# Optimization experiments

Measured on AMD Instinct MI355X. Metric: run time of the kernel, lower is better.

The kernel has to match this reference:

```python
import jax, jax.numpy as jnp
import numpy as np

NUM_HEADS = 8
KEY_DIM = 16
D_V = 32  # attn_ratio * key_dim


def _conv1x1_bn(x, w, s, b):
    # x: [B, Cin, H, W], w: [Cout, Cin]; 1x1 conv == channel contraction,
    # eval-mode BatchNorm folded into per-channel scale s and bias b.
    y = jnp.einsum('bchw,oc->bohw', x, w)
    return y * s[:, None, None] + b[:, None, None]


def setup_inputs() -> dict:
    key = jax.random.key(0)
    ks = jax.random.split(key, 14)
    B, C, H, W = 16, 256, 32, 32
    nh_kd, dh = NUM_HEADS * KEY_DIM, NUM_HEADS * D_V
    f = jax.random.normal
    return {
        'x': f(ks[0], (B, C, H, W), jnp.float32),
        'wq': f(ks[1], (nh_kd, C), jnp.float32) * 0.05,
        'sq': jax.random.uniform(ks[2], (nh_kd,), jnp.float32),
        'bq': f(ks[3], (nh_kd,), jnp.float32) * 0.05,
        'wk': f(ks[4], (nh_kd, C), jnp.float32) * 0.05,
        'sk': jax.random.uniform(ks[5], (nh_kd,), jnp.float32),
        'bk': f(ks[6], (nh_kd,), jnp.float32) * 0.05,
        'wv': f(ks[7], (dh, C), jnp.float32) * 0.05,
        'sv': jax.random.uniform(ks[8], (dh,), jnp.float32),
        'bv': f(ks[9], (dh,), jnp.float32) * 0.05,
        'wp': f(ks[10], (C, dh), jnp.float32) * 0.05,
        'sp': jax.random.uniform(ks[11], (C,), jnp.float32),
        'bp': f(ks[12], (C,), jnp.float32) * 0.05,
    }


def reference(x, wq, sq, bq, wk, sk, bk, wv, sv, bv, wp, sp, bp):
    B, C, H, W = x.shape
    N = H * W
    # QKV projections (1x1 conv + folded BN)
    q = _conv1x1_bn(x, wq, sq, bq).reshape(B, NUM_HEADS, KEY_DIM, N)  # b h k n
    k = _conv1x1_bn(x, wk, sk, bk).reshape(B, NUM_HEADS, KEY_DIM, N)  # b h k m
    v = _conv1x1_bn(x, wv, sv, bv).reshape(B, NUM_HEADS, D_V, N)      # b h d m
    # NOTE: the original forward does NOT apply self.scale to the scores.
    attn = jnp.einsum('bhkn,bhkm->bhnm', q, k)
    attn = jax.nn.softmax(attn, axis=-1)
    out = jnp.einsum('bhnm,bhdm->bhdn', attn, v)  # b h d n
    out = out.reshape(B, NUM_HEADS * D_V, H, W)
    # proj = Sequential(activation, Conv2d_BN): activation FIRST
    out = jax.nn.relu(out)
    return _conv1x1_bn(out, wp, sp, bp)
```

## Files before the change

### kernel.cpp

```cpp
#include <hip/hip_runtime.h>

#define NTOT 1024
#define CIN  256
#define BATCH 16
#define NH   8
#define KD   16
#define DV   32
#define L2E  1.44269504088896340736f

typedef unsigned short u16;
typedef unsigned int   u32;
typedef __attribute__((ext_vector_type(2)))  _Float16 f16x2;
typedef __attribute__((ext_vector_type(8)))  _Float16 f16x8;
typedef __attribute__((ext_vector_type(16))) float    f32x16;

__device__ inline f16x8 as_f16x8(uint4 u) { return __builtin_bit_cast(f16x8, u); }
__device__ inline f16x2 as_f16x2(u32 u)   { return __builtin_bit_cast(f16x2, u); }
__device__ inline u32 pkrtz(float a, float b) {
  return __builtin_bit_cast(u32, __builtin_amdgcn_cvt_pkrtz(a, b));
}
__device__ inline u16 f2h(float x) {
  return __builtin_bit_cast(u16, (_Float16)x);
}
__device__ inline float fexp2(float x) {
#if __has_builtin(__builtin_amdgcn_exp2f)
  return __builtin_amdgcn_exp2f(x);
#else
  float r; asm("v_exp_f32 %0, %1" : "=v"(r) : "v"(x)); return r;
#endif
}
__device__ inline float dot2acc(u32 p2, float c) {
#if __has_builtin(__builtin_amdgcn_fdot2)
  const f16x2 one2 = __builtin_bit_cast(f16x2, (u32)0x3C003C00u);
  return __builtin_amdgcn_fdot2(as_f16x2(p2), one2, c, false);
#else
  const f16x2 v = as_f16x2(p2);
  return c + (float)v[0] + (float)v[1];
#endif
}

__global__ __launch_bounds__(256) void prep_fused(
    const float* __restrict__ X, u16* __restrict__ Xt,
    const float* __restrict__ wq, const float* __restrict__ sq, const float* __restrict__ bq,
    const float* __restrict__ wk, const float* __restrict__ sk, const float* __restrict__ bk,
    const float* __restrict__ wv, const float* __restrict__ sv, const float* __restrict__ bv,
    const float* __restrict__ wp, const float* __restrict__ sp, const float* __restrict__ bp,
    u16* __restrict__ wqkv, u16* __restrict__ wph, float* __restrict__ ball)
{
  __shared__ u16 T[64][64];
  const int bx = blockIdx.x;
  const int t  = threadIdx.x;
  if (bx < 1024) {
    const int n0 = (bx & 15) * 64;
    const int c0 = ((bx >> 4) & 3) * 64;
    const int b  = bx >> 6;
    #pragma unroll
    for (int rr = 0; rr < 4; ++rr) {
      const int c  = rr*16 + (t>>4);
      const int n4 = (t&15)*4;
      const float4 v = *(const float4*)&X[((size_t)b*CIN + c0 + c)*NTOT + n0 + n4];
      ushort4 r; r.x=f2h(v.x); r.y=f2h(v.y); r.z=f2h(v.z); r.w=f2h(v.w);
      *(ushort4*)&T[c][n4] = r;
    }
    __syncthreads();
    const int nl = t & 63;
    #pragma unroll
    for (int j = 0; j < 2; ++j) {
      const int oct = (t>>6)*2 + j;
      uint4 w;
      w.x = (u32)T[oct*8+0][nl] | ((u32)T[oct*8+1][nl] << 16);
      w.y = (u32)T[oct*8+2][nl] | ((u32)T[oct*8+3][nl] << 16);
      w.z = (u32)T[oct*8+4][nl] | ((u32)T[oct*8+5][nl] << 16);
      w.w = (u32)T[oct*8+6][nl] | ((u32)T[oct*8+7][nl] << 16);
      *(uint4*)&Xt[((size_t)b*NTOT + n0 + nl)*CIN + c0 + oct*8] = w;
    }
  } else {
    const int row = (bx - 1024)*4 + (t>>6);
    const int ln  = t & 63;
    const float* src; u16* dst; float sc, bi;
    if (row < 128)      { src = wq + (size_t)row*CIN;       sc = sq[row]*L2E;     bi = bq[row]*L2E;     dst = wqkv + (size_t)row*CIN; }
    else if (row < 256) { src = wk + (size_t)(row-128)*CIN; sc = sk[row-128];     bi = bk[row-128];     dst = wqkv + (size_t)row*CIN; }
    else if (row < 512) { src = wv + (size_t)(row-256)*CIN; sc = sv[row-256];     bi = bv[row-256];     dst = wqkv + (size_t)row*CIN; }
    else                { src = wp + (size_t)(row-512)*CIN; sc = sp[row-512];     bi = bp[row-512];     dst = wph + (size_t)(row-512)*CIN; }
    const float4 v = *(const float4*)&src[ln*4];
    ushort4 r;
    r.x = f2h(v.x*sc); r.y = f2h(v.y*sc); r.z = f2h(v.z*sc); r.w = f2h(v.w*sc);
    *(ushort4*)&dst[ln*4] = r;
    if (ln == 0) ball[row] = bi;
  }
}

template<int BN, int MODE>
__global__ __launch_bounds__(256) void conv_mfma(
    const u16* __restrict__ Wh, const u16* __restrict__ Bt,
    const float* __restrict__ ball,
    u16* __restrict__ q_t, u16* __restrict__ k_t, u16* __restrict__ v_h,
    float* __restrict__ outp)
{
  constexpr int FN = BN / 64;
  constexpr int NB = BN / 32;
  __shared__ u16 A_lds[2][128 * 64];
  __shared__ u16 B_lds[2][BN * 64];
  const int t    = threadIdx.x;
  const int lane = t & 63;
  const int w    = t >> 6;
  const int wm = w >> 1, wn = w & 1;
  const int g = lane >> 5, nl = lane & 31;
  const int n0 = blockIdx.x * BN;
  const int m0 = blockIdx.y * 128;
  const int b  = blockIdx.z;

  f32x16 acc[2][FN] = {};
  uint4 rA[4], rB[NB];

  #pragma unroll
  for (int r = 0; r < 4; ++r) {
    const int idx = t + r*256, row = idx >> 3, ch = idx & 7;
    rA[r] = *(const uint4*)&Wh[(size_t)(m0+row)*CIN + ch*8];
  }
  #pragma unroll
  for (int r = 0; r < NB; ++r) {
    const int idx = t + r*256, row = idx >> 3, ch = idx & 7;
    rB[r] = *(const uint4*)&Bt[((size_t)b*NTOT + n0 + row)*CIN + ch*8];
  }
  #pragma unroll
  for (int r = 0; r < 4; ++r) {
    const int idx = t + r*256, row = idx >> 3, ch = idx & 7;
    *(uint4*)&A_lds[0][row*64 + ((ch ^ (row&7))*8)] = rA[r];
  }
  #pragma unroll
  for (int r = 0; r < NB; ++r) {
    const int idx = t + r*256, row = idx >> 3, ch = idx & 7;
    *(uint4*)&B_lds[0][row*64 + ((ch ^ (row&7))*8)] = rB[r];
  }
  __syncthreads();

  for (int it = 0; it < 4; ++it) {
    const int cur = it & 1;
    if (it < 3) {
      const int c0 = (it+1)*64;
      #pragma unroll
      for (int r = 0; r < 4; ++r) {
        const int idx = t + r*256, row = idx >> 3, ch = idx & 7;
        rA[r] = *(const uint4*)&Wh[(size_t)(m0+row)*CIN + c0 + ch*8];
      }
      #pragma unroll
      for (int r = 0; r < NB; ++r) {
        const int idx = t + r*256, row = idx >> 3, ch = idx & 7;
        rB[r] = *(const uint4*)&Bt[((size_t)b*NTOT + n0 + row)*CIN + c0 + ch*8];
      }
    }
    #pragma unroll
    for (int ks = 0; ks < 4; ++ks) {
      const int ch = 2*ks + g;
      f16x8 a[2], bb[FN];
      #pragma unroll
      for (int fi = 0; fi < 2; ++fi) {
        const int row = wm*64 + fi*32 + nl;
        a[fi] = as_f16x8(*(const uint4*)&A_lds[cur][row*64 + ((ch ^ (row&7))*8)]);
      }
      #pragma unroll
      for (int fj = 0; fj < FN; ++fj) {
        const int row = wn*(BN/2) + fj*32 + nl;
        bb[fj] = as_f16x8(*(const uint4*)&B_lds[cur][row*64 + ((ch ^ (row&7))*8)]);
      }
      #pragma unroll
      for (int fi = 0; fi < 2; ++fi)
        #pragma unroll
        for (int fj = 0; fj < FN; ++fj)
          acc[fi][fj] = __builtin_amdgcn_mfma_f32_32x32x16_f16(a[fi], bb[fj], acc[fi][fj], 0, 0, 0);
    }
    if (it < 3) {
      #pragma unroll
      for (int r = 0; r < 4; ++r) {
        const int idx = t + r*256, row = idx >> 3, ch = idx & 7;
        *(uint4*)&A_lds[cur^1][row*64 + ((ch ^ (row&7))*8)] = rA[r];
      }
      #pragma unroll
      for (int r = 0; r < NB; ++r) {
        const int idx = t + r*256, row = idx >> 3, ch = idx & 7;
        *(uint4*)&B_lds[cur^1][row*64 + ((ch ^ (row&7))*8)] = rB[r];
      }
      __syncthreads();
    }
  }

  #pragma unroll
  for (int fi = 0; fi < 2; ++fi) {
    #pragma unroll
    for (int fj = 0; fj < FN; ++fj) {
      const int n = n0 + wn*(BN/2) + fj*32 + nl;
      #pragma unroll
      for (int q = 0; q < 4; ++q) {
        const int ob = m0 + wm*64 + fi*32 + 8*q + 4*g;
        const float v0 = acc[fi][fj][4*q+0] + ball[ob+0];
        const float v1 = acc[fi][fj][4*q+1] + ball[ob+1];
        const float v2 = acc[fi][fj][4*q+2] + ball[ob+2];
        const float v3 = acc[fi][fj][4*q+3] + ball[ob+3];
        if (MODE == 0) {
          if (ob < 128) {
            const int h = ob >> 4, k0 = ob & 15;
            ushort4 r; r.x = f2h(v0); r.y = f2h(v1); r.z = f2h(v2); r.w = f2h(v3);
            *(ushort4*)&q_t[(((size_t)b*NH + h)*NTOT + n)*KD + k0] = r;
          } else if (ob < 256) {
            const int oo = ob - 128;
            const int h = oo >> 4, k0 = oo & 15;
            const int plane = k0 >> 3, j0 = k0 & 7;
            ushort4 r; r.x = f2h(v0); r.y = f2h(v1); r.z = f2h(v2); r.w = f2h(v3);
            *(ushort4*)&k_t[((((size_t)b*NH + h)*2 + plane)*NTOT + n)*8 + j0] = r;
          } else {
            const int oo = ob - 256;
            const int h = oo >> 5, d0 = oo & 31;
            const int mb = n >> 4, loc = n & 15;
            const int g2 = (loc >> 2) & 1;
            const int j  = (loc & 3) + ((loc >> 3) << 2);
            u16* vp = v_h + (((((size_t)b*NH + h)*64 + mb)*2 + g2)*32 + d0)*8 + j;
            vp[0*8] = f2h(v0);
            vp[1*8] = f2h(v1);
            vp[2*8] = f2h(v2);
            vp[3*8] = f2h(v3);
          }
        } else {
          float* op = outp + ((size_t)b*CIN + ob)*NTOT + n;
          op[0*NTOT] = v0; op[1*NTOT] = v1; op[2*NTOT] = v2; op[3*NTOT] = v3;
        }
      }
    }
  }
}

__global__ __launch_bounds__(1024) void attn_mfma(
    const u16* __restrict__ Qt,
    const u16* __restrict__ Kt,
    const u16* __restrict__ Vt,
    u16* __restrict__ Ot)
{
  __shared__ u16 K_lds[2*NTOT*8];
  __shared__ u16 V_lds[4096*8];
  const int t    = threadIdx.x;
  const int lane = t & 63;
  const int wave = t >> 6;
  const int bh   = blockIdx.x >> 1;
  const int half = blockIdx.x & 1;
  const int g = lane >> 5, nl = lane & 31;
  const int n0 = half*512 + wave*32;

  const u16* Kh = Kt + (size_t)bh*(2*NTOT*8);
  const u16* Vh = Vt + (size_t)bh*(4096*8);
  const u16* Qh = Qt + (size_t)bh*(NTOT*KD);

  #pragma unroll
  for (int r = 0; r < 2; ++r) {
    const int uu = r*1024 + t;
    *(uint4*)&K_lds[uu*8] = *(const uint4*)&Kh[uu*8];
  }
  #pragma unroll
  for (int r = 0; r < 4; ++r) {
    const int uu = r*1024 + t;
    *(uint4*)&V_lds[uu*8] = *(const uint4*)&Vh[uu*8];
  }

  const f16x8 qf = as_f16x8(*(const uint4*)&Qh[(size_t)(n0+nl)*KD + g*8]);
  __syncthreads();

  const f32x16 fzero = {};
  f32x16 acc = {};
  float l = 0.f;
  const char* Kb = (const char*)K_lds + g*16384 + nl*16;
  const char* Vb = (const char*)V_lds + g*512   + nl*16;

  f16x8 kf  = as_f16x8(*(const uint4*)(Kb));
  uint4 va0 = *(const uint4*)(Vb);
  uint4 va1 = *(const uint4*)(Vb + 1024);
  f32x16 s_cur = __builtin_amdgcn_mfma_f32_32x32x16_f16(kf, qf, fzero, 0, 0, 0);

  #pragma unroll 2
  for (int st = 0; st < 31; ++st) {
    const f16x8 kfn = as_f16x8(*(const uint4*)(Kb + (st+1)*512));
    __builtin_amdgcn_s_setprio(1);
    const f32x16 s_next = __builtin_amdgcn_mfma_f32_32x32x16_f16(kfn, qf, fzero, 0, 0, 0);
    __builtin_amdgcn_s_setprio(0);
    const uint4 nva0 = *(const uint4*)(Vb + (st+1)*2048);
    const uint4 nva1 = *(const uint4*)(Vb + (st+1)*2048 + 1024);

    float p[16];
    #pragma unroll
    for (int r = 0; r < 16; ++r) p[r] = fexp2(s_cur[r]);
    uint4 b0, b1;
    b0.x = pkrtz(p[0],  p[1]);  b0.y = pkrtz(p[2],  p[3]);
    b0.z = pkrtz(p[4],  p[5]);  b0.w = pkrtz(p[6],  p[7]);
    b1.x = pkrtz(p[8],  p[9]);  b1.y = pkrtz(p[10], p[11]);
    b1.z = pkrtz(p[12], p[13]); b1.w = pkrtz(p[14], p[15]);
    l = dot2acc(b0.x, l); l = dot2acc(b0.y, l);
    l = dot2acc(b0.z, l); l = dot2acc(b0.w, l);
    l = dot2acc(b1.x, l); l = dot2acc(b1.y, l);
    l = dot2acc(b1.z, l); l = dot2acc(b1.w, l);

    __builtin_amdgcn_s_setprio(1);
    acc = __builtin_amdgcn_mfma_f32_32x32x16_f16(as_f16x8(va0), as_f16x8(b0), acc, 0, 0, 0);
    acc = __builtin_amdgcn_mfma_f32_32x32x16_f16(as_f16x8(va1), as_f16x8(b1), acc, 0, 0, 0);
    __builtin_amdgcn_s_setprio(0);
    s_cur = s_next; va0 = nva0; va1 = nva1;
  }
  {
    float p[16];
    #pragma unroll
    for (int r = 0; r < 16; ++r) p[r] = fexp2(s_cur[r]);
    uint4 b0, b1;
    b0.x = pkrtz(p[0],  p[1]);  b0.y = pkrtz(p[2],  p[3]);
    b0.z = pkrtz(p[4],  p[5]);  b0.w = pkrtz(p[6],  p[7]);
    b1.x = pkrtz(p[8],  p[9]);  b1.y = pkrtz(p[10], p[11]);
    b1.z = pkrtz(p[12], p[13]); b1.w = pkrtz(p[14], p[15]);
    l = dot2acc(b0.x, l); l = dot2acc(b0.y, l);
    l = dot2acc(b0.z, l); l = dot2acc(b0.w, l);
    l = dot2acc(b1.x, l); l = dot2acc(b1.y, l);
    l = dot2acc(b1.z, l); l = dot2acc(b1.w, l);
    acc = __builtin_amdgcn_mfma_f32_32x32x16_f16(as_f16x8(va0), as_f16x8(b0), acc, 0, 0, 0);
    acc = __builtin_amdgcn_mfma_f32_32x32x16_f16(as_f16x8(va1), as_f16x8(b1), acc, 0, 0, 0);
  }

  const float lt = l + __shfl_xor(l, 32);
  const float rl = 1.0f / lt;
  const int b = bh >> 3, h = bh & 7;
  u16* op = Ot + ((size_t)b*NTOT + n0 + nl)*CIN + h*DV;
  #pragma unroll
  for (int q = 0; q < 4; ++q) {
    const float v0 = fmaxf(acc[4*q+0]*rl, 0.f);
    const float v1 = fmaxf(acc[4*q+1]*rl, 0.f);
    const float v2 = fmaxf(acc[4*q+2]*rl, 0.f);
    const float v3 = fmaxf(acc[4*q+3]*rl, 0.f);
    uint2 pk; pk.x = pkrtz(v0, v1); pk.y = pkrtz(v2, v3);
    *(uint2*)&op[8*q + 4*g] = pk;
  }
}

extern "C" void kernel_launch(void* const* d_in, const int* in_sizes, int n_in,
                              void* d_out, int out_size, void* d_ws, size_t ws_size,
                              hipStream_t stream) {
  const float* x  = (const float*)d_in[0];
  const float* wq = (const float*)d_in[1];
  const float* sq = (const float*)d_in[2];
  const float* bq = (const float*)d_in[3];
  const float* wk = (const float*)d_in[4];
  const float* sk = (const float*)d_in[5];
  const float* bk = (const float*)d_in[6];
  const float* wv = (const float*)d_in[7];
  const float* sv = (const float*)d_in[8];
  const float* bv = (const float*)d_in[9];
  const float* wp = (const float*)d_in[10];
  const float* sp = (const float*)d_in[11];
  const float* bp = (const float*)d_in[12];
  float* out = (float*)d_out;

  char* ws = (char*)d_ws;
  u16*   x_t  = (u16*)(ws);
  u16*   q_t  = (u16*)(ws + (8u  << 20));
  u16*   k_t  = (u16*)(ws + (12u << 20));
  u16*   v_h  = (u16*)(ws + (16u << 20));
  u16*   wqkv = (u16*)(ws + (24u << 20));
  u16*   wph  = (u16*)(ws + (24u << 20) + (256u << 10));
  float* ball = (float*)(ws + (24u << 20) + (384u << 10));

  prep_fused<<<dim3(1216), dim3(256), 0, stream>>>(
      x, x_t, wq, sq, bq, wk, sk, bk, wv, sv, bv, wp, sp, bp, wqkv, wph, ball);
  conv_mfma<128, 0><<<dim3(8, 4, 16), dim3(256), 0, stream>>>(
      wqkv, x_t, ball, q_t, k_t, v_h, nullptr);
  attn_mfma<<<dim3(256), dim3(1024), 0, stream>>>(q_t, k_t, v_h, x_t );
  conv_mfma<64, 1><<<dim3(16, 2, 16), dim3(256), 0, stream>>>(
      wph, x_t , ball + 512, nullptr, nullptr, nullptr, out);
}
```

Before: 57.08 us.

## Split attention keys across wave pairs and stream V through double-buffered LDS

The attention kernel now launches 1024 blocks of 512 threads instead of 256 blocks of 1024. Each block covers 128 queries, and the key range is split between two wave groups whose partial accumulators and row sums are merged through LDS at the end. V is no longer loaded whole up front. It is staged chunk by chunk into a double-buffered LDS area with a barrier per chunk, which shrinks LDS use so more blocks can be resident and lets loading overlap with compute. The row sum also uses four independent accumulators to shorten the dependency chain. The cost is that K is reloaded four times more often overall, plus extra barriers and a final reduction step.

Result: slower. 102.6 us (+79.7%).

```diff
diff --git a/kernel.cpp b/kernel.cpp
--- a/kernel.cpp
+++ b/kernel.cpp
@@ -229,108 +229,121 @@
   }
 }
 
-__global__ __launch_bounds__(1024) void attn_mfma(
+#define ATTN_STEP(SLOC, DO_NEXT, DO_KF)                                  \
+  {                                                                      \
+    const uint4 va0 = *(const uint4*)&vbuf[((SLOC)&1)*1024 + g*256 + nl*8];       \
+    const uint4 va1 = *(const uint4*)&vbuf[((SLOC)&1)*1024 + 512 + g*256 + nl*8]; \
+    f32x16 s_next;                                                       \
+    if (DO_NEXT) {                                                       \
+      __builtin_amdgcn_s_setprio(1);                                     \
+      s_next = __builtin_amdgcn_mfma_f32_32x32x16_f16(kf, qf, fzero, 0, 0, 0); \
+      __builtin_amdgcn_s_setprio(0);                                     \
+    }                                                                    \
+    if (DO_KF) kf = as_f16x8(*(const uint4*)(Kb + ((SLOC)+2)*512));      \
+    float p[16];                                                         \
+    _Pragma("unroll")                                                    \
+    for (int r = 0; r < 16; ++r) p[r] = fexp2(s_cur[r]);                 \
+    uint4 pb0, pb1;                                                      \
+    pb0.x = pkrtz(p[0],  p[1]);  pb0.y = pkrtz(p[2],  p[3]);             \
+    pb0.z = pkrtz(p[4],  p[5]);  pb0.w = pkrtz(p[6],  p[7]);             \
+    pb1.x = pkrtz(p[8],  p[9]);  pb1.y = pkrtz(p[10], p[11]);            \
+    pb1.z = pkrtz(p[12], p[13]); pb1.w = pkrtz(p[14], p[15]);            \
+    l0 = dot2acc(pb0.x, l0); l1 = dot2acc(pb0.y, l1);                    \
+    l2 = dot2acc(pb0.z, l2); l3 = dot2acc(pb0.w, l3);                    \
+    l0 = dot2acc(pb1.x, l0); l1 = dot2acc(pb1.y, l1);                    \
+    l2 = dot2acc(pb1.z, l2); l3 = dot2acc(pb1.w, l3);                    \
+    __builtin_amdgcn_s_setprio(1);                                       \
+    acc = __builtin_amdgcn_mfma_f32_32x32x16_f16(as_f16x8(va0), as_f16x8(pb0), acc, 0, 0, 0); \
+    acc = __builtin_amdgcn_mfma_f32_32x32x16_f16(as_f16x8(va1), as_f16x8(pb1), acc, 0, 0, 0); \
+    __builtin_amdgcn_s_setprio(0);                                       \
+    if (DO_NEXT) s_cur = s_next;                                         \
+  }
+
+__global__ __launch_bounds__(512, 6) void attn_mfma(
     const u16* __restrict__ Qt,
     const u16* __restrict__ Kt,
     const u16* __restrict__ Vt,
     u16* __restrict__ Ot)
 {
   __shared__ u16 K_lds[2*NTOT*8];
-  __shared__ u16 V_lds[4096*8];
+  __shared__ u16 V_lds[2][2][2048];
   const int t    = threadIdx.x;
   const int lane = t & 63;
-  const int wave = t >> 6;
-  const int bh   = blockIdx.x >> 1;
-  const int half = blockIdx.x & 1;
+  const int w    = t >> 6;
+  const int qg   = w & 3;
+  const int mh   = w >> 2;
+  const int bh    = blockIdx.x >> 3;
+  const int qpart = blockIdx.x & 7;
   const int g = lane >> 5, nl = lane & 31;
-  const int n0 = half*512 + wave*32;
+  const int n0 = qpart*128 + qg*32;
 
   const u16* Kh = Kt + (size_t)bh*(2*NTOT*8);
   const u16* Vh = Vt + (size_t)bh*(4096*8);
   const u16* Qh = Qt + (size_t)bh*(NTOT*KD);
 
   #pragma unroll
-  for (int r = 0; r < 2; ++r) {
-    const int uu = r*1024 + t;
+  for (int r = 0; r < 4; ++r) {
+    const int uu = r*512 + t;
     *(uint4*)&K_lds[uu*8] = *(const uint4*)&Kh[uu*8];
   }
-  #pragma unroll
-  for (int r = 0; r < 4; ++r) {
-    const int uu = r*1024 + t;
-    *(uint4*)&V_lds[uu*8] = *(const uint4*)&Vh[uu*8];
-  }
+  const int sh   = t >> 8;
+  const int sidx = t & 255;
+  const u16* Vsrc = Vh + sh*16384 + sidx*8;
+  *(uint4*)&V_lds[sh][0][sidx*8] = *(const uint4*)(Vsrc);
 
   const f16x8 qf = as_f16x8(*(const uint4*)&Qh[(size_t)(n0+nl)*KD + g*8]);
   __syncthreads();
 
   const f32x16 fzero = {};
   f32x16 acc = {};
-  float l = 0.f;
-  const char* Kb = (const char*)K_lds + g*16384 + nl*16;
-  const char* Vb = (const char*)V_lds + g*512   + nl*16;
-
-  f16x8 kf  = as_f16x8(*(const uint4*)(Kb));
-  uint4 va0 = *(const uint4*)(Vb);
-  uint4 va1 = *(const uint4*)(Vb + 1024);
+  float l0 = 0.f, l1 = 0.f, l2 = 0.f, l3 = 0.f;
+  const char* Kb = (const char*)K_lds + g*16384 + mh*8192 + nl*16;
+
+  f16x8 kf = as_f16x8(*(const uint4*)(Kb));
   f32x16 s_cur = __builtin_amdgcn_mfma_f32_32x32x16_f16(kf, qf, fzero, 0, 0, 0);
-
-  #pragma unroll 2
-  for (int st = 0; st < 31; ++st) {
-    const f16x8 kfn = as_f16x8(*(const uint4*)(Kb + (st+1)*512));
-    __builtin_amdgcn_s_setprio(1);
-    const f32x16 s_next = __builtin_amdgcn_mfma_f32_32x32x16_f16(kfn, qf, fzero, 0, 0, 0);
-    __builtin_amdgcn_s_setprio(0);
-    const uint4 nva0 = *(const uint4*)(Vb + (st+1)*2048);
-    const uint4 nva1 = *(const uint4*)(Vb + (st+1)*2048 + 1024);
-
-    float p[16];
-    #pragma unroll
-    for (int r = 0; r < 16; ++r) p[r] = fexp2(s_cur[r]);
-    uint4 b0, b1;
-    b0.x = pkrtz(p[0],  p[1]);  b0.y = pkrtz(p[2],  p[3]);
-    b0.z = pkrtz(p[4],  p[5]);  b0.w = pkrtz(p[6],  p[7]);
-    b1.x = pkrtz(p[8],  p[9]);  b1.y = pkrtz(p[10], p[11]);
-    b1.z = pkrtz(p[12], p[13]); b1.w = pkrtz(p[14], p[15]);
-    l = dot2acc(b0.x, l); l = dot2acc(b0.y, l);
-    l = dot2acc(b0.z, l); l = dot2acc(b0.w, l);
-    l = dot2acc(b1.x, l); l = dot2acc(b1.y, l);
-    l = dot2acc(b1.z, l); l = dot2acc(b1.w, l);
-
-    __builtin_amdgcn_s_setprio(1);
-    acc = __builtin_amdgcn_mfma_f32_32x32x16_f16(as_f16x8(va0), as_f16x8(b0), acc, 0, 0, 0);
-    acc = __builtin_amdgcn_mfma_f32_32x32x16_f16(as_f16x8(va1), as_f16x8(b1), acc, 0, 0, 0);
-    __builtin_amdgcn_s_setprio(0);
-    s_cur = s_next; va0 = nva0; va1 = nva1;
+  kf = as_f16x8(*(const uint4*)(Kb + 512));
+
+  for (int c = 0; c < 7; ++c) {
+    const uint4 vstage = *(const uint4*)(Vsrc + (size_t)(c+1)*2048);
+    const u16* vbuf = &V_lds[mh][c & 1][0];
+    ATTN_STEP(2*c,     true, true);
+    ATTN_STEP(2*c + 1, true, true);
+    *(uint4*)&V_lds[sh][(c & 1) ^ 1][sidx*8] = vstage;
+    __syncthreads();
   }
   {
-    float p[16];
-    #pragma unroll
-    for (int r = 0; r < 16; ++r) p[r] = fexp2(s_cur[r]);
-    uint4 b0, b1;
-    b0.x = pkrtz(p[0],  p[1]);  b0.y = pkrtz(p[2],  p[3]);
-    b0.z = pkrtz(p[4],  p[5]);  b0.w = pkrtz(p[6],  p[7]);
-    b1.x = pkrtz(p[8],  p[9]);  b1.y = pkrtz(p[10], p[11]);
-    b1.z = pkrtz(p[12], p[13]); b1.w = pkrtz(p[14], p[15]);
-    l = dot2acc(b0.x, l); l = dot2acc(b0.y, l);
-    l = dot2acc(b0.z, l); l = dot2acc(b0.w, l);
-    l = dot2acc(b1.x, l); l = dot2acc(b1.y, l);
-    l = dot2acc(b1.z, l); l = dot2acc(b1.w, l);
-    acc = __builtin_amdgcn_mfma_f32_32x32x16_f16(as_f16x8(va0), as_f16x8(b0), acc, 0, 0, 0);
-    acc = __builtin_amdgcn_mfma_f32_32x32x16_f16(as_f16x8(va1), as_f16x8(b1), acc, 0, 0, 0);
-  }
-
-  const float lt = l + __shfl_xor(l, 32);
-  const float rl = 1.0f / lt;
-  const int b = bh >> 3, h = bh & 7;
-  u16* op = Ot + ((size_t)b*NTOT + n0 + nl)*CIN + h*DV;
-  #pragma unroll
-  for (int q = 0; q < 4; ++q) {
-    const float v0 = fmaxf(acc[4*q+0]*rl, 0.f);
-    const float v1 = fmaxf(acc[4*q+1]*rl, 0.f);
-    const float v2 = fmaxf(acc[4*q+2]*rl, 0.f);
-    const float v3 = fmaxf(acc[4*q+3]*rl, 0.f);
-    uint2 pk; pk.x = pkrtz(v0, v1); pk.y = pkrtz(v2, v3);
-    *(uint2*)&op[8*q + 4*g] = pk;
+    const u16* vbuf = &V_lds[mh][1][0];
+    ATTN_STEP(14, true,  false);
+    ATTN_STEP(15, false, false);
+  }
+
+  __syncthreads();
+  float* M = (float*)K_lds;
+  const int mo = qg * 1088;
+  const float lp = (l0 + l1) + (l2 + l3);
+  if (mh == 0) {
+    #pragma unroll
+    for (int r = 0; r < 16; ++r) M[mo + r*64 + lane] = acc[r];
+    M[mo + 1024 + lane] = lp;
+  }
+  __syncthreads();
+  if (mh == 1) {
+    #pragma unroll
+    for (int r = 0; r < 16; ++r) acc[r] += M[mo + r*64 + lane];
+    const float lsum = lp + M[mo + 1024 + lane];
+    const float lt = lsum + __shfl_xor(lsum, 32);
+    const float rl = 1.0f / lt;
+    const int b = bh >> 3, h = bh & 7;
+    u16* op = Ot + ((size_t)b*NTOT + n0 + nl)*CIN + h*DV;
+    #pragma unroll
+    for (int q = 0; q < 4; ++q) {
+      const float v0 = fmaxf(acc[4*q+0]*rl, 0.f);
+      const float v1 = fmaxf(acc[4*q+1]*rl, 0.f);
+      const float v2 = fmaxf(acc[4*q+2]*rl, 0.f);
+      const float v3 = fmaxf(acc[4*q+3]*rl, 0.f);
+      uint2 pk; pk.x = pkrtz(v0, v1); pk.y = pkrtz(v2, v3);
+      *(uint2*)&op[8*q + 4*g] = pk;
+    }
   }
 }
 
@@ -365,7 +378,7 @@
       x, x_t, wq, sq, bq, wk, sk, bk, wv, sv, bv, wp, sp, bp, wqkv, wph, ball);
   conv_mfma<128, 0><<<dim3(8, 4, 16), dim3(256), 0, stream>>>(
       wqkv, x_t, ball, q_t, k_t, v_h, nullptr);
-  attn_mfma<<<dim3(256), dim3(1024), 0, stream>>>(q_t, k_t, v_h, x_t );
+  attn_mfma<<<dim3(1024), dim3(512), 0, stream>>>(q_t, k_t, v_h, x_t );
   conv_mfma<64, 1><<<dim3(16, 2, 16), dim3(256), 0, stream>>>(
       wph, x_t , ball + 512, nullptr, nullptr, nullptr, out);
 }
```

## Fuse X transpose into QKV conv, restructure attention loop, remap blocks

Applied to the files above, without the earlier changes.

Removes the separate fp32→fp16 transpose of X by having the QKV conv read X directly and scatter-convert it into swizzled LDS, dropping a global round trip for the transposed copy. The conv loses its register double-buffering and now uses single-buffered LDS with scalar 16-bit LDS stores. The attention kernel is restructured into a two-stream unrolled loop with four independent row-sum accumulators to expose more MFMA/exp overlap, and its block index is remapped so that consecutive blocks span different batch-heads. The weight prep becomes its own small kernel.

New measurement: 133.9 us. 2.35x slower.

```diff
diff --git a/kernel.cpp b/kernel.cpp
--- a/kernel.cpp
+++ b/kernel.cpp
@@ -39,157 +39,93 @@
 #endif
 }
 
-__global__ __launch_bounds__(256) void prep_fused(
-    const float* __restrict__ X, u16* __restrict__ Xt,
+__global__ __launch_bounds__(64) void prep_weights(
     const float* __restrict__ wq, const float* __restrict__ sq, const float* __restrict__ bq,
     const float* __restrict__ wk, const float* __restrict__ sk, const float* __restrict__ bk,
     const float* __restrict__ wv, const float* __restrict__ sv, const float* __restrict__ bv,
     const float* __restrict__ wp, const float* __restrict__ sp, const float* __restrict__ bp,
     u16* __restrict__ wqkv, u16* __restrict__ wph, float* __restrict__ ball)
 {
-  __shared__ u16 T[64][64];
-  const int bx = blockIdx.x;
-  const int t  = threadIdx.x;
-  if (bx < 1024) {
-    const int n0 = (bx & 15) * 64;
-    const int c0 = ((bx >> 4) & 3) * 64;
-    const int b  = bx >> 6;
-    #pragma unroll
-    for (int rr = 0; rr < 4; ++rr) {
-      const int c  = rr*16 + (t>>4);
-      const int n4 = (t&15)*4;
-      const float4 v = *(const float4*)&X[((size_t)b*CIN + c0 + c)*NTOT + n0 + n4];
-      ushort4 r; r.x=f2h(v.x); r.y=f2h(v.y); r.z=f2h(v.z); r.w=f2h(v.w);
-      *(ushort4*)&T[c][n4] = r;
-    }
-    __syncthreads();
-    const int nl = t & 63;
-    #pragma unroll
-    for (int j = 0; j < 2; ++j) {
-      const int oct = (t>>6)*2 + j;
-      uint4 w;
-      w.x = (u32)T[oct*8+0][nl] | ((u32)T[oct*8+1][nl] << 16);
-      w.y = (u32)T[oct*8+2][nl] | ((u32)T[oct*8+3][nl] << 16);
-      w.z = (u32)T[oct*8+4][nl] | ((u32)T[oct*8+5][nl] << 16);
-      w.w = (u32)T[oct*8+6][nl] | ((u32)T[oct*8+7][nl] << 16);
-      *(uint4*)&Xt[((size_t)b*NTOT + n0 + nl)*CIN + c0 + oct*8] = w;
-    }
-  } else {
-    const int row = (bx - 1024)*4 + (t>>6);
-    const int ln  = t & 63;
-    const float* src; u16* dst; float sc, bi;
-    if (row < 128)      { src = wq + (size_t)row*CIN;       sc = sq[row]*L2E;     bi = bq[row]*L2E;     dst = wqkv + (size_t)row*CIN; }
-    else if (row < 256) { src = wk + (size_t)(row-128)*CIN; sc = sk[row-128];     bi = bk[row-128];     dst = wqkv + (size_t)row*CIN; }
-    else if (row < 512) { src = wv + (size_t)(row-256)*CIN; sc = sv[row-256];     bi = bv[row-256];     dst = wqkv + (size_t)row*CIN; }
-    else                { src = wp + (size_t)(row-512)*CIN; sc = sp[row-512];     bi = bp[row-512];     dst = wph + (size_t)(row-512)*CIN; }
-    const float4 v = *(const float4*)&src[ln*4];
-    ushort4 r;
-    r.x = f2h(v.x*sc); r.y = f2h(v.y*sc); r.z = f2h(v.z*sc); r.w = f2h(v.w*sc);
-    *(ushort4*)&dst[ln*4] = r;
-    if (ln == 0) ball[row] = bi;
-  }
-}
-
-template<int BN, int MODE>
-__global__ __launch_bounds__(256) void conv_mfma(
-    const u16* __restrict__ Wh, const u16* __restrict__ Bt,
+  const int row = blockIdx.x;
+  const int t = threadIdx.x;
+  const float* src; u16* dst; float sc, bi;
+  if (row < 128)      { src = wq + (size_t)row*CIN;       sc = sq[row]*L2E;     bi = bq[row]*L2E;     dst = wqkv + (size_t)row*CIN; }
+  else if (row < 256) { src = wk + (size_t)(row-128)*CIN; sc = sk[row-128];     bi = bk[row-128];     dst = wqkv + (size_t)row*CIN; }
+  else if (row < 512) { src = wv + (size_t)(row-256)*CIN; sc = sv[row-256];     bi = bv[row-256];     dst = wqkv + (size_t)row*CIN; }
+  else                { src = wp + (size_t)(row-512)*CIN; sc = sp[row-512];     bi = bp[row-512];     dst = wph + (size_t)(row-512)*CIN; }
+  const float4 v = *(const float4*)&src[t*4];
+  ushort4 r;
+  r.x = f2h(v.x*sc); r.y = f2h(v.y*sc); r.z = f2h(v.z*sc); r.w = f2h(v.w*sc);
+  *(ushort4*)&dst[t*4] = r;
+  if (t == 0) ball[row] = bi;
+}
+
+__global__ __launch_bounds__(256) void conv_qkv(
+    const float* __restrict__ X, const u16* __restrict__ Wh,
     const float* __restrict__ ball,
-    u16* __restrict__ q_t, u16* __restrict__ k_t, u16* __restrict__ v_h,
-    float* __restrict__ outp)
+    u16* __restrict__ q_t, u16* __restrict__ k_t, u16* __restrict__ v_h)
 {
-  constexpr int FN = BN / 64;
-  constexpr int NB = BN / 32;
-  __shared__ u16 A_lds[2][128 * 64];
-  __shared__ u16 B_lds[2][BN * 64];
+  __shared__ u16 A_lds[128 * 64];
+  __shared__ u16 B_lds[128 * 64];
   const int t    = threadIdx.x;
   const int lane = t & 63;
   const int w    = t >> 6;
   const int wm = w >> 1, wn = w & 1;
   const int g = lane >> 5, nl = lane & 31;
-  const int n0 = blockIdx.x * BN;
+  const int n0 = blockIdx.x * 128;
   const int m0 = blockIdx.y * 128;
   const int b  = blockIdx.z;
 
-  f32x16 acc[2][FN] = {};
-  uint4 rA[4], rB[NB];
-
-  #pragma unroll
-  for (int r = 0; r < 4; ++r) {
-    const int idx = t + r*256, row = idx >> 3, ch = idx & 7;
-    rA[r] = *(const uint4*)&Wh[(size_t)(m0+row)*CIN + ch*8];
-  }
-  #pragma unroll
-  for (int r = 0; r < NB; ++r) {
-    const int idx = t + r*256, row = idx >> 3, ch = idx & 7;
-    rB[r] = *(const uint4*)&Bt[((size_t)b*NTOT + n0 + row)*CIN + ch*8];
-  }
-  #pragma unroll
-  for (int r = 0; r < 4; ++r) {
-    const int idx = t + r*256, row = idx >> 3, ch = idx & 7;
-    *(uint4*)&A_lds[0][row*64 + ((ch ^ (row&7))*8)] = rA[r];
-  }
-  #pragma unroll
-  for (int r = 0; r < NB; ++r) {
-    const int idx = t + r*256, row = idx >> 3, ch = idx & 7;
-    *(uint4*)&B_lds[0][row*64 + ((ch ^ (row&7))*8)] = rB[r];
-  }
-  __syncthreads();
-
-  for (int it = 0; it < 4; ++it) {
-    const int cur = it & 1;
-    if (it < 3) {
-      const int c0 = (it+1)*64;
-      #pragma unroll
-      for (int r = 0; r < 4; ++r) {
-        const int idx = t + r*256, row = idx >> 3, ch = idx & 7;
-        rA[r] = *(const uint4*)&Wh[(size_t)(m0+row)*CIN + c0 + ch*8];
-      }
-      #pragma unroll
-      for (int r = 0; r < NB; ++r) {
-        const int idx = t + r*256, row = idx >> 3, ch = idx & 7;
-        rB[r] = *(const uint4*)&Bt[((size_t)b*NTOT + n0 + row)*CIN + c0 + ch*8];
-      }
-    }
+  f32x16 acc[2][2] = {};
+
+  for (int c0 = 0; c0 < CIN; c0 += 64) {
+    #pragma unroll
+    for (int r = 0; r < 4; ++r) {
+      const int idx = t + r*256, row = idx >> 3, ch = idx & 7;
+      *(uint4*)&A_lds[row*64 + ((ch ^ (row&7))*8)] =
+          *(const uint4*)&Wh[(size_t)(m0+row)*CIN + c0 + ch*8];
+    }
+    #pragma unroll
+    for (int r = 0; r < 8; ++r) {
+      const int idx = t + r*256;
+      const int c  = idx >> 5;
+      const int nq = (idx & 31) * 4;
+      const float4 v = *(const float4*)&X[((size_t)b*CIN + c0 + c)*NTOT + n0 + nq];
+      const int ch = c >> 3, cl = c & 7;
+      B_lds[(nq+0)*64 + ((ch ^ ((nq+0)&7))*8) + cl] = f2h(v.x);
+      B_lds[(nq+1)*64 + ((ch ^ ((nq+1)&7))*8) + cl] = f2h(v.y);
+      B_lds[(nq+2)*64 + ((ch ^ ((nq+2)&7))*8) + cl] = f2h(v.z);
+      B_lds[(nq+3)*64 + ((ch ^ ((nq+3)&7))*8) + cl] = f2h(v.w);
+    }
+    __syncthreads();
     #pragma unroll
     for (int ks = 0; ks < 4; ++ks) {
       const int ch = 2*ks + g;
-      f16x8 a[2], bb[FN];
+      f16x8 a[2], bb[2];
       #pragma unroll
       for (int fi = 0; fi < 2; ++fi) {
         const int row = wm*64 + fi*32 + nl;
-        a[fi] = as_f16x8(*(const uint4*)&A_lds[cur][row*64 + ((ch ^ (row&7))*8)]);
-      }
-      #pragma unroll
-      for (int fj = 0; fj < FN; ++fj) {
-        const int row = wn*(BN/2) + fj*32 + nl;
-        bb[fj] = as_f16x8(*(const uint4*)&B_lds[cur][row*64 + ((ch ^ (row&7))*8)]);
+        a[fi] = as_f16x8(*(const uint4*)&A_lds[row*64 + ((ch ^ (row&7))*8)]);
+      }
+      #pragma unroll
+      for (int fj = 0; fj < 2; ++fj) {
+        const int row = wn*64 + fj*32 + nl;
+        bb[fj] = as_f16x8(*(const uint4*)&B_lds[row*64 + ((ch ^ (row&7))*8)]);
       }
       #pragma unroll
       for (int fi = 0; fi < 2; ++fi)
         #pragma unroll
-        for (int fj = 0; fj < FN; ++fj)
+        for (int fj = 0; fj < 2; ++fj)
           acc[fi][fj] = __builtin_amdgcn_mfma_f32_32x32x16_f16(a[fi], bb[fj], acc[fi][fj], 0, 0, 0);
     }
-    if (it < 3) {
-      #pragma unroll
-      for (int r = 0; r < 4; ++r) {
-        const int idx = t + r*256, row = idx >> 3, ch = idx & 7;
-        *(uint4*)&A_lds[cur^1][row*64 + ((ch ^ (row&7))*8)] = rA[r];
-      }
-      #pragma unroll
-      for (int r = 0; r < NB; ++r) {
-        const int idx = t + r*256, row = idx >> 3, ch = idx & 7;
-        *(uint4*)&B_lds[cur^1][row*64 + ((ch ^ (row&7))*8)] = rB[r];
-      }
-      __syncthreads();
-    }
+    __syncthreads();
   }
 
   #pragma unroll
   for (int fi = 0; fi < 2; ++fi) {
     #pragma unroll
-    for (int fj = 0; fj < FN; ++fj) {
-      const int n = n0 + wn*(BN/2) + fj*32 + nl;
+    for (int fj = 0; fj < 2; ++fj) {
+      const int n = n0 + wn*64 + fj*32 + nl;
       #pragma unroll
       for (int q = 0; q < 4; ++q) {
         const int ob = m0 + wm*64 + fi*32 + 8*q + 4*g;
@@ -197,34 +133,131 @@
         const float v1 = acc[fi][fj][4*q+1] + ball[ob+1];
         const float v2 = acc[fi][fj][4*q+2] + ball[ob+2];
         const float v3 = acc[fi][fj][4*q+3] + ball[ob+3];
-        if (MODE == 0) {
-          if (ob < 128) {
-            const int h = ob >> 4, k0 = ob & 15;
-            ushort4 r; r.x = f2h(v0); r.y = f2h(v1); r.z = f2h(v2); r.w = f2h(v3);
-            *(ushort4*)&q_t[(((size_t)b*NH + h)*NTOT + n)*KD + k0] = r;
-          } else if (ob < 256) {
-            const int oo = ob - 128;
-            const int h = oo >> 4, k0 = oo & 15;
-            const int plane = k0 >> 3, j0 = k0 & 7;
-            ushort4 r; r.x = f2h(v0); r.y = f2h(v1); r.z = f2h(v2); r.w = f2h(v3);
-            *(ushort4*)&k_t[((((size_t)b*NH + h)*2 + plane)*NTOT + n)*8 + j0] = r;
-          } else {
-            const int oo = ob - 256;
-            const int h = oo >> 5, d0 = oo & 31;
-            const int mb = n >> 4, loc = n & 15;
-            const int g2 = (loc >> 2) & 1;
-            const int j  = (loc & 3) + ((loc >> 3) << 2);
-            u16* vp = v_h + (((((size_t)b*NH + h)*64 + mb)*2 + g2)*32 + d0)*8 + j;
-            vp[0*8] = f2h(v0);
-            vp[1*8] = f2h(v1);
-            vp[2*8] = f2h(v2);
-            vp[3*8] = f2h(v3);
-          }
+        if (ob < 128) {
+          const int h = ob >> 4, k0 = ob & 15;
+          ushort4 r; r.x = f2h(v0); r.y = f2h(v1); r.z = f2h(v2); r.w = f2h(v3);
+          *(ushort4*)&q_t[(((size_t)b*NH + h)*NTOT + n)*KD + k0] = r;
+        } else if (ob < 256) {
+          const int oo = ob - 128;
+          const int h = oo >> 4, k0 = oo & 15;
+          const int plane = k0 >> 3, j0 = k0 & 7;
+          ushort4 r; r.x = f2h(v0); r.y = f2h(v1); r.z = f2h(v2); r.w = f2h(v3);
+          *(ushort4*)&k_t[((((size_t)b*NH + h)*2 + plane)*NTOT + n)*8 + j0] = r;
         } else {
-          float* op = outp + ((size_t)b*CIN + ob)*NTOT + n;
-          op[0*NTOT] = v0; op[1*NTOT] = v1; op[2*NTOT] = v2; op[3*NTOT] = v3;
+          const int oo = ob - 256;
+          const int h = oo >> 5, d0 = oo & 31;
+          const int mb = n >> 4, loc = n & 15;
+          const int g2 = (loc >> 2) & 1;
+          const int j  = (loc & 3) + ((loc >> 3) << 2);
+          u16* vp = v_h + (((((size_t)b*NH + h)*64 + mb)*2 + g2)*32 + d0)*8 + j;
+          vp[0*8] = f2h(v0);
+          vp[1*8] = f2h(v1);
+          vp[2*8] = f2h(v2);
+          vp[3*8] = f2h(v3);
         }
       }
+    }
+  }
+}
+
+__global__ __launch_bounds__(256) void conv_out(
+    const u16* __restrict__ Wh, const u16* __restrict__ Bt,
+    const float* __restrict__ ball, float* __restrict__ outp)
+{
+  __shared__ u16 A_lds[2][128 * 64];
+  __shared__ u16 B_lds[2][64 * 64];
+  const int t    = threadIdx.x;
+  const int lane = t & 63;
+  const int w    = t >> 6;
+  const int wm = w >> 1, wn = w & 1;
+  const int g = lane >> 5, nl = lane & 31;
+  const int n0 = blockIdx.x * 64;
+  const int m0 = blockIdx.y * 128;
+  const int b  = blockIdx.z;
+
+  f32x16 acc[2][1] = {};
+  uint4 rA[4], rB[2];
+
+  #pragma unroll
+  for (int r = 0; r < 4; ++r) {
+    const int idx = t + r*256, row = idx >> 3, ch = idx & 7;
+    rA[r] = *(const uint4*)&Wh[(size_t)(m0+row)*CIN + ch*8];
+  }
+  #pragma unroll
+  for (int r = 0; r < 2; ++r) {
+    const int idx = t + r*256, row = idx >> 3, ch = idx & 7;
+    rB[r] = *(const uint4*)&Bt[((size_t)b*NTOT + n0 + row)*CIN + ch*8];
+  }
+  #pragma unroll
+  for (int r = 0; r < 4; ++r) {
+    const int idx = t + r*256, row = idx >> 3, ch = idx & 7;
+    *(uint4*)&A_lds[0][row*64 + ((ch ^ (row&7))*8)] = rA[r];
+  }
+  #pragma unroll
+  for (int r = 0; r < 2; ++r) {
+    const int idx = t + r*256, row = idx >> 3, ch = idx & 7;
+    *(uint4*)&B_lds[0][row*64 + ((ch ^ (row&7))*8)] = rB[r];
+  }
+  __syncthreads();
+
+  for (int it = 0; it < 4; ++it) {
+    const int cur = it & 1;
+    if (it < 3) {
+      const int c0 = (it+1)*64;
+      #pragma unroll
+      for (int r = 0; r < 4; ++r) {
+        const int idx = t + r*256, row = idx >> 3, ch = idx & 7;
+        rA[r] = *(const uint4*)&Wh[(size_t)(m0+row)*CIN + c0 + ch*8];
+      }
+      #pragma unroll
+      for (int r = 0; r < 2; ++r) {
+        const int idx = t + r*256, row = idx >> 3, ch = idx & 7;
+        rB[r] = *(const uint4*)&Bt[((size_t)b*NTOT + n0 + row)*CIN + c0 + ch*8];
+      }
+    }
+    #pragma unroll
+    for (int ks = 0; ks < 4; ++ks) {
+      const int ch = 2*ks + g;
+      f16x8 a[2], bb;
+      #pragma unroll
+      for (int fi = 0; fi < 2; ++fi) {
+        const int row = wm*64 + fi*32 + nl;
+        a[fi] = as_f16x8(*(const uint4*)&A_lds[cur][row*64 + ((ch ^ (row&7))*8)]);
+      }
+      {
+        const int row = wn*32 + nl;
+        bb = as_f16x8(*(const uint4*)&B_lds[cur][row*64 + ((ch ^ (row&7))*8)]);
+      }
+      #pragma unroll
+      for (int fi = 0; fi < 2; ++fi)
+        acc[fi][0] = __builtin_amdgcn_mfma_f32_32x32x16_f16(a[fi], bb, acc[fi][0], 0, 0, 0);
+    }
+    if (it < 3) {
+      #pragma unroll
+      for (int r = 0; r < 4; ++r) {
+        const int idx = t + r*256, row = idx >> 3, ch = idx & 7;
+        *(uint4*)&A_lds[cur^1][row*64 + ((ch ^ (row&7))*8)] = rA[r];
+      }
+      #pragma unroll
+      for (int r = 0; r < 2; ++r) {
+        const int idx = t + r*256, row = idx >> 3, ch = idx & 7;
+        *(uint4*)&B_lds[cur^1][row*64 + ((ch ^ (row&7))*8)] = rB[r];
+      }
+      __syncthreads();
+    }
+  }
+
+  #pragma unroll
+  for (int fi = 0; fi < 2; ++fi) {
+    const int n = n0 + wn*32 + nl;
+    #pragma unroll
+    for (int q = 0; q < 4; ++q) {
+      const int ob = m0 + wm*64 + fi*32 + 8*q + 4*g;
+      float* op = outp + ((size_t)b*CIN + ob)*NTOT + n;
+      op[0*NTOT] = acc[fi][0][4*q+0] + ball[ob+0];
+      op[1*NTOT] = acc[fi][0][4*q+1] + ball[ob+1];
+      op[2*NTOT] = acc[fi][0][4*q+2] + ball[ob+2];
+      op[3*NTOT] = acc[fi][0][4*q+3] + ball[ob+3];
     }
   }
 }
@@ -240,8 +273,10 @@
   const int t    = threadIdx.x;
   const int lane = t & 63;
   const int wave = t >> 6;
-  const int bh   = blockIdx.x >> 1;
-  const int half = blockIdx.x & 1;
+  const int bid  = blockIdx.x;
+  const int wgid = (bid & 7)*32 + (bid >> 3);
+  const int bh   = wgid >> 1;
+  const int half = wgid & 1;
   const int g = lane >> 5, nl = lane & 31;
   const int n0 = half*512 + wave*32;
 
@@ -265,61 +300,75 @@
 
   const f32x16 fzero = {};
   f32x16 acc = {};
-  float l = 0.f;
+  float l0 = 0.f, l1 = 0.f, l2 = 0.f, l3 = 0.f;
   const char* Kb = (const char*)K_lds + g*16384 + nl*16;
   const char* Vb = (const char*)V_lds + g*512   + nl*16;
 
-  f16x8 kf  = as_f16x8(*(const uint4*)(Kb));
-  uint4 va0 = *(const uint4*)(Vb);
-  uint4 va1 = *(const uint4*)(Vb + 1024);
-  f32x16 s_cur = __builtin_amdgcn_mfma_f32_32x32x16_f16(kf, qf, fzero, 0, 0, 0);
-
-  #pragma unroll 2
-  for (int st = 0; st < 31; ++st) {
-    const f16x8 kfn = as_f16x8(*(const uint4*)(Kb + (st+1)*512));
-    __builtin_amdgcn_s_setprio(1);
-    const f32x16 s_next = __builtin_amdgcn_mfma_f32_32x32x16_f16(kfn, qf, fzero, 0, 0, 0);
-    __builtin_amdgcn_s_setprio(0);
-    const uint4 nva0 = *(const uint4*)(Vb + (st+1)*2048);
-    const uint4 nva1 = *(const uint4*)(Vb + (st+1)*2048 + 1024);
-
-    float p[16];
-    #pragma unroll
-    for (int r = 0; r < 16; ++r) p[r] = fexp2(s_cur[r]);
-    uint4 b0, b1;
-    b0.x = pkrtz(p[0],  p[1]);  b0.y = pkrtz(p[2],  p[3]);
-    b0.z = pkrtz(p[4],  p[5]);  b0.w = pkrtz(p[6],  p[7]);
-    b1.x = pkrtz(p[8],  p[9]);  b1.y = pkrtz(p[10], p[11]);
-    b1.z = pkrtz(p[12], p[13]); b1.w = pkrtz(p[14], p[15]);
-    l = dot2acc(b0.x, l); l = dot2acc(b0.y, l);
-    l = dot2acc(b0.z, l); l = dot2acc(b0.w, l);
-    l = dot2acc(b1.x, l); l = dot2acc(b1.y, l);
-    l = dot2acc(b1.z, l); l = dot2acc(b1.w, l);
-
-    __builtin_amdgcn_s_setprio(1);
-    acc = __builtin_amdgcn_mfma_f32_32x32x16_f16(as_f16x8(va0), as_f16x8(b0), acc, 0, 0, 0);
-    acc = __builtin_amdgcn_mfma_f32_32x32x16_f16(as_f16x8(va1), as_f16x8(b1), acc, 0, 0, 0);
-    __builtin_amdgcn_s_setprio(0);
-    s_cur = s_next; va0 = nva0; va1 = nva1;
-  }
-  {
-    float p[16];
-    #pragma unroll
-    for (int r = 0; r < 16; ++r) p[r] = fexp2(s_cur[r]);
-    uint4 b0, b1;
-    b0.x = pkrtz(p[0],  p[1]);  b0.y = pkrtz(p[2],  p[3]);
-    b0.z = pkrtz(p[4],  p[5]);  b0.w = pkrtz(p[6],  p[7]);
-    b1.x = pkrtz(p[8],  p[9]);  b1.y = pkrtz(p[10], p[11]);
-    b1.z = pkrtz(p[12], p[13]); b1.w = pkrtz(p[14], p[15]);
-    l = dot2acc(b0.x, l); l = dot2acc(b0.y, l);
-    l = dot2acc(b0.z, l); l = dot2acc(b0.w, l);
-    l = dot2acc(b1.x, l); l = dot2acc(b1.y, l);
-    l = dot2acc(b1.z, l); l = dot2acc(b1.w, l);
-    acc = __builtin_amdgcn_mfma_f32_32x32x16_f16(as_f16x8(va0), as_f16x8(b0), acc, 0, 0, 0);
-    acc = __builtin_amdgcn_mfma_f32_32x32x16_f16(as_f16x8(va1), as_f16x8(b1), acc, 0, 0, 0);
-  }
-
-  const float lt = l + __shfl_xor(l, 32);
+  f16x8 kfA = as_f16x8(*(const uint4*)(Kb));
+  f16x8 kfB = as_f16x8(*(const uint4*)(Kb + 512));
+  f32x16 sA = __builtin_amdgcn_mfma_f32_32x32x16_f16(kfA, qf, fzero, 0, 0, 0);
+  f32x16 sB = __builtin_amdgcn_mfma_f32_32x32x16_f16(kfB, qf, fzero, 0, 0, 0);
+  kfA = as_f16x8(*(const uint4*)(Kb + 1024));
+  kfB = as_f16x8(*(const uint4*)(Kb + 1536));
+  uint4 vaA0 = *(const uint4*)(Vb);
+  uint4 vaA1 = *(const uint4*)(Vb + 1024);
+  uint4 vaB0 = *(const uint4*)(Vb + 2048);
+  uint4 vaB1 = *(const uint4*)(Vb + 3072);
+
+  #pragma unroll
+  for (int i = 0; i < 16; ++i) {
+    {
+      float p[16];
+      #pragma unroll
+      for (int r = 0; r < 16; ++r) p[r] = fexp2(sA[r]);
+      uint4 pb0, pb1;
+      pb0.x = pkrtz(p[0],  p[1]);  pb0.y = pkrtz(p[2],  p[3]);
+      pb0.z = pkrtz(p[4],  p[5]);  pb0.w = pkrtz(p[6],  p[7]);
+      pb1.x = pkrtz(p[8],  p[9]);  pb1.y = pkrtz(p[10], p[11]);
+      pb1.z = pkrtz(p[12], p[13]); pb1.w = pkrtz(p[14], p[15]);
+      l0 = dot2acc(pb0.x, l0); l1 = dot2acc(pb0.y, l1);
+      l2 = dot2acc(pb0.z, l2); l3 = dot2acc(pb0.w, l3);
+      l0 = dot2acc(pb1.x, l0); l1 = dot2acc(pb1.y, l1);
+      l2 = dot2acc(pb1.z, l2); l3 = dot2acc(pb1.w, l3);
+      if (i < 15) sA = __builtin_amdgcn_mfma_f32_32x32x16_f16(kfA, qf, fzero, 0, 0, 0);
+      if (i < 14) kfA = as_f16x8(*(const uint4*)(Kb + (2*i+4)*512));
+      __builtin_amdgcn_s_setprio(1);
+      acc = __builtin_amdgcn_mfma_f32_32x32x16_f16(as_f16x8(vaA0), as_f16x8(pb0), acc, 0, 0, 0);
+      acc = __builtin_amdgcn_mfma_f32_32x32x16_f16(as_f16x8(vaA1), as_f16x8(pb1), acc, 0, 0, 0);
+      __builtin_amdgcn_s_setprio(0);
+      if (i < 15) {
+        vaA0 = *(const uint4*)(Vb + (2*i+2)*2048);
+        vaA1 = *(const uint4*)(Vb + (2*i+2)*2048 + 1024);
+      }
+    }
+    {
+      float p[16];
+      #pragma unroll
+      for (int r = 0; r < 16; ++r) p[r] = fexp2(sB[r]);
+      uint4 pb0, pb1;
+      pb0.x = pkrtz(p[0],  p[1]);  pb0.y = pkrtz(p[2],  p[3]);
+      pb0.z = pkrtz(p[4],  p[5]);  pb0.w = pkrtz(p[6],  p[7]);
+      pb1.x = pkrtz(p[8],  p[9]);  pb1.y = pkrtz(p[10], p[11]);
+      pb1.z = pkrtz(p[12], p[13]); pb1.w = pkrtz(p[14], p[15]);
+      l0 = dot2acc(pb0.x, l0); l1 = dot2acc(pb0.y, l1);
+      l2 = dot2acc(pb0.z, l2); l3 = dot2acc(pb0.w, l3);
+      l0 = dot2acc(pb1.x, l0); l1 = dot2acc(pb1.y, l1);
+      l2 = dot2acc(pb1.z, l2); l3 = dot2acc(pb1.w, l3);
+      if (i < 15) sB = __builtin_amdgcn_mfma_f32_32x32x16_f16(kfB, qf, fzero, 0, 0, 0);
+      if (i < 14) kfB = as_f16x8(*(const uint4*)(Kb + (2*i+5)*512));
+      __builtin_amdgcn_s_setprio(1);
+      acc = __builtin_amdgcn_mfma_f32_32x32x16_f16(as_f16x8(vaB0), as_f16x8(pb0), acc, 0, 0, 0);
+      acc = __builtin_amdgcn_mfma_f32_32x32x16_f16(as_f16x8(vaB1), as_f16x8(pb1), acc, 0, 0, 0);
+      __builtin_amdgcn_s_setprio(0);
+      if (i < 15) {
+        vaB0 = *(const uint4*)(Vb + (2*i+3)*2048);
+        vaB1 = *(const uint4*)(Vb + (2*i+3)*2048 + 1024);
+      }
+    }
+  }
+
+  const float lp = (l0 + l1) + (l2 + l3);
+  const float lt = lp + __shfl_xor(lp, 32);
   const float rl = 1.0f / lt;
   const int b = bh >> 3, h = bh & 7;
   u16* op = Ot + ((size_t)b*NTOT + n0 + nl)*CIN + h*DV;
@@ -353,7 +402,7 @@
   float* out = (float*)d_out;
 
   char* ws = (char*)d_ws;
-  u16*   x_t  = (u16*)(ws);
+  u16*   o_t  = (u16*)(ws);
   u16*   q_t  = (u16*)(ws + (8u  << 20));
   u16*   k_t  = (u16*)(ws + (12u << 20));
   u16*   v_h  = (u16*)(ws + (16u << 20));
@@ -361,11 +410,11 @@
   u16*   wph  = (u16*)(ws + (24u << 20) + (256u << 10));
   float* ball = (float*)(ws + (24u << 20) + (384u << 10));
 
-  prep_fused<<<dim3(1216), dim3(256), 0, stream>>>(
-      x, x_t, wq, sq, bq, wk, sk, bk, wv, sv, bv, wp, sp, bp, wqkv, wph, ball);
-  conv_mfma<128, 0><<<dim3(8, 4, 16), dim3(256), 0, stream>>>(
-      wqkv, x_t, ball, q_t, k_t, v_h, nullptr);
-  attn_mfma<<<dim3(256), dim3(1024), 0, stream>>>(q_t, k_t, v_h, x_t );
-  conv_mfma<64, 1><<<dim3(16, 2, 16), dim3(256), 0, stream>>>(
-      wph, x_t , ball + 512, nullptr, nullptr, nullptr, out);
-}
+  prep_weights<<<dim3(768), dim3(64), 0, stream>>>(
+      wq, sq, bq, wk, sk, bk, wv, sv, bv, wp, sp, bp, wqkv, wph, ball);
+  conv_qkv<<<dim3(8, 4, 16), dim3(256), 0, stream>>>(
+      x, wqkv, ball, q_t, k_t, v_h);
+  attn_mfma<<<dim3(256), dim3(1024), 0, stream>>>(q_t, k_t, v_h, o_t);
+  conv_out<<<dim3(16, 2, 16), dim3(256), 0, stream>>>(
+      wph, o_t, ball + 512, out);
+}
```
